# Performance work log

Hardware: AMD Instinct MI355X
Metric: run time of the kernel (lower is better)

The kernel has to match this reference:

```python
import jax, jax.numpy as jnp
import numpy as np
import math

NUM_HEADS = 16
D_MODEL = 1024
B, T = 1, 4096


def setup_inputs() -> dict:
    key = jax.random.key(0)
    kx, kq, kk, kv, ko = jax.random.split(key, 5)
    s = 1.0 / math.sqrt(D_MODEL)
    return {
        "x": jax.random.normal(kx, (B, T, D_MODEL), dtype=jnp.float32),
        "Wq": jax.random.normal(kq, (D_MODEL, D_MODEL), dtype=jnp.float32) * s,
        "Wk": jax.random.normal(kk, (D_MODEL, D_MODEL), dtype=jnp.float32) * s,
        "Wv": jax.random.normal(kv, (D_MODEL, D_MODEL), dtype=jnp.float32) * s,
        "Wo": jax.random.normal(ko, (D_MODEL, D_MODEL), dtype=jnp.float32) * s,
    }


def reference(x, Wq, Wk, Wv, Wo):
    # x: (B, T, D); weights stored torch-Linear style: y = x @ W.T
    Bx, Tx, D = x.shape
    H = NUM_HEADS
    dk = D // H
    q = (x @ Wq.T).reshape(Bx, Tx, H, dk)  # (B,T,H,dk)
    k = (x @ Wk.T).reshape(Bx, Tx, H, dk)
    v = (x @ Wv.T).reshape(Bx, Tx, H, dk)
    # scores: (B,H,T,T), scaled dot-product
    scores = jnp.einsum("bthd,bshd->bhts", q, k) / math.sqrt(dk)
    causal_mask = jnp.triu(jnp.ones((Tx, Tx), dtype=bool), k=1)  # True above diag
    scores = jnp.where(causal_mask, jnp.float32(-jnp.inf), scores).astype(jnp.float32)
    attn = jax.nn.softmax(scores, axis=-1)  # fp32 softmax, as in the torch module
    out = jnp.einsum("bhts,bshd->bthd", attn, v).reshape(Bx, Tx, D)
    return out @ Wo.T
```

## Files before the change

### kernel.cpp

```cpp
#include <hip/hip_runtime.h>
#include <hip/hip_bf16.h>
#include <math.h>

typedef __attribute__((ext_vector_type(8)))  __bf16 bf16x8;
typedef __attribute__((ext_vector_type(4)))  __bf16 bf16x4;
typedef __attribute__((ext_vector_type(4)))  float  f32x4;
typedef __attribute__((ext_vector_type(16))) float  f32x16;

static constexpr int T_SEQ = 4096;
static constexpr int DM    = 1024;
static constexpr int NH    = 16;
static constexpr int C2_QB    = 22;
static constexpr int C3_QB    = 44;
static constexpr int SPL_ROWS = T_SEQ - C2_QB * 64;
static constexpr int C3_ROWS  = T_SEQ - C3_QB * 64;
static constexpr int NY = 126;
static constexpr float QSCALE = 0.125f * 1.44269504088896340736f;
static constexpr float FIXED_M = 10.0f;

__device__ __forceinline__ void gload16(const void* g, void* l) {
    __builtin_amdgcn_global_load_lds(
        (const __attribute__((address_space(1))) unsigned int*)g,
        (__attribute__((address_space(3))) unsigned int*)l,
        16, 0, 0);
}

__device__ __forceinline__ unsigned cvtpk_bf16(float a, float b) {
    unsigned r;
    asm("v_cvt_pk_bf16_f32 %0, %1, %2" : "=v"(r) : "v"(a), "v"(b));
    return r;
}
__device__ __forceinline__ void permswap(unsigned& x, unsigned& y) {
    asm("v_permlane32_swap_b32 %0, %1" : "+v"(x), "+v"(y));
}
__device__ __forceinline__ float xhalf_sum(float v) {
    union { float f; unsigned u; } a, b;
    a.f = v; b.f = v;
    asm volatile("" : "+v"(b.u));
    permswap(a.u, b.u);
    return a.f + b.f;
}

__global__ __launch_bounds__(256)
void cvt_bf16(const float* __restrict__ in, __bf16* __restrict__ out, int n4) {
    int i = blockIdx.x * blockDim.x + threadIdx.x;
    if (i >= n4) return;
    float4 v = ((const float4*)in)[i];
    bf16x4 o;
    o[0] = (__bf16)v.x; o[1] = (__bf16)v.y; o[2] = (__bf16)v.z; o[3] = (__bf16)v.w;
    ((bf16x4*)out)[i] = o;
}

__global__ __launch_bounds__(256)
void cvt4_bf16(const float* __restrict__ a0, const float* __restrict__ a1,
               const float* __restrict__ a2, const float* __restrict__ a3,
               __bf16* __restrict__ o0, __bf16* __restrict__ o1,
               __bf16* __restrict__ o2, __bf16* __restrict__ o3, int n4) {
    int i = blockIdx.x * blockDim.x + threadIdx.x;
    if (i >= n4) return;
    const float* in = blockIdx.y == 0 ? a0 : blockIdx.y == 1 ? a1 : blockIdx.y == 2 ? a2 : a3;
    __bf16* out     = blockIdx.y == 0 ? o0 : blockIdx.y == 1 ? o1 : blockIdx.y == 2 ? o2 : o3;
    float4 v = ((const float4*)in)[i];
    bf16x4 o;
    o[0] = (__bf16)v.x; o[1] = (__bf16)v.y; o[2] = (__bf16)v.z; o[3] = (__bf16)v.w;
    ((bf16x4*)out)[i] = o;
}

template<bool OUT_BF16>
__device__ __forceinline__ void gemm_body(const __bf16* __restrict__ A,
                                          const __bf16* __restrict__ B,
                                          void* __restrict__ Cout,
                                          int N, int K, float scale,
                                          int bx, int by) {
    __shared__ __align__(16) __bf16 Al[128 * 64];
    __shared__ __align__(16) __bf16 Bl[128 * 64];
    const int tid  = threadIdx.x;
    const int lane = tid & 63;
    const int wid  = tid >> 6;
    const int wr   = wid >> 1, wc = wid & 1;
    const int m0   = by * 128, n0 = bx * 128;
    const int r    = lane & 15, g = lane >> 4;

    f32x4 acc[4][4];
    const f32x4 z4 = {0.f, 0.f, 0.f, 0.f};
    #pragma unroll
    for (int i = 0; i < 4; ++i)
        #pragma unroll
        for (int j = 0; j < 4; ++j) acc[i][j] = z4;

    for (int kt = 0; kt < K; kt += 64) {
        __syncthreads();
        #pragma unroll
        for (int p = 0; p < 4; ++p) {
            int u    = p * 256 + tid;
            int row  = u >> 3;
            int col8 = (u & 7) ^ (row & 7);
            gload16(A + (size_t)(m0 + row) * K + kt + col8 * 8,
                    (char*)Al + (p * 256 + wid * 64) * 16);
            gload16(B + (size_t)(n0 + row) * K + kt + col8 * 8,
                    (char*)Bl + (p * 256 + wid * 64) * 16);
        }
        __syncthreads();
        __builtin_amdgcn_s_setprio(1);
        #pragma unroll
        for (int kk = 0; kk < 2; ++kk) {
            bf16x8 af[4], bfr[4];
            #pragma unroll
            for (int mi = 0; mi < 4; ++mi)
                af[mi] = *(const bf16x8*)&Al[(wr * 64 + mi * 16 + r) * 64 + (((kk * 4 + g) ^ (r & 7)) * 8)];
            #pragma unroll
            for (int nj = 0; nj < 4; ++nj)
                bfr[nj] = *(const bf16x8*)&Bl[(wc * 64 + nj * 16 + r) * 64 + (((kk * 4 + g) ^ (r & 7)) * 8)];
            #pragma unroll
            for (int mi = 0; mi < 4; ++mi)
                #pragma unroll
                for (int nj = 0; nj < 4; ++nj)
                    acc[mi][nj] = __builtin_amdgcn_mfma_f32_16x16x32_bf16(af[mi], bfr[nj], acc[mi][nj], 0, 0, 0);
        }
        __builtin_amdgcn_s_setprio(0);
    }
    #pragma unroll
    for (int mi = 0; mi < 4; ++mi)
        #pragma unroll
        for (int nj = 0; nj < 4; ++nj)
            #pragma unroll
            for (int j = 0; j < 4; ++j) {
                int row = m0 + wr * 64 + mi * 16 + g * 4 + j;
                int col = n0 + wc * 64 + nj * 16 + r;
                float v = acc[mi][nj][j] * scale;
                if (OUT_BF16) ((__bf16*)Cout)[(size_t)row * N + col] = (__bf16)v;
                else          ((float*)Cout)[(size_t)row * N + col]  = v;
            }
}

__global__ __launch_bounds__(256)
void gemm_qkv(const __bf16* __restrict__ A,
              const __bf16* __restrict__ W0, const __bf16* __restrict__ W1,
              const __bf16* __restrict__ W2,
              __bf16* __restrict__ O0, __bf16* __restrict__ O1, __bf16* __restrict__ O2) {
    const int z = blockIdx.z;
    const __bf16* B = z == 0 ? W0 : (z == 1 ? W1 : W2);
    __bf16*       C = z == 0 ? O0 : (z == 1 ? O1 : O2);
    float scale = z == 0 ? QSCALE : 1.0f;
    gemm_body<true>(A, B, C, DM, DM, scale, blockIdx.x, blockIdx.y);
}

__global__ __launch_bounds__(256)
void gemm_out(const __bf16* __restrict__ A, const __bf16* __restrict__ B,
              float* __restrict__ C) {
    gemm_body<false>(A, B, C, DM, DM, 1.0f, blockIdx.x, blockIdx.y);
}

__global__ __launch_bounds__(256)
void vtrans(const __bf16* __restrict__ V, __bf16* __restrict__ Vt) {
    __shared__ __bf16 tl[64][72];
    const int tid = threadIdx.x;
    const int t0  = blockIdx.x * 64;
    const int h   = blockIdx.y;
    #pragma unroll
    for (int p = 0; p < 2; ++p) {
        int c = p * 256 + tid, row = c >> 3, col8 = c & 7;
        *(bf16x8*)&tl[row][col8 * 8] =
            *(const bf16x8*)(V + (size_t)(t0 + row) * DM + h * 64 + col8 * 8);
    }
    __syncthreads();
    #pragma unroll
    for (int p = 0; p < 2; ++p) {
        int c = p * 256 + tid, d = c >> 3, tc8 = c & 7;
        bf16x8 o;
        #pragma unroll
        for (int e = 0; e < 8; ++e) o[e] = tl[tc8 * 8 + e][d];
        *(bf16x8*)(Vt + (size_t)(h * 64 + d) * T_SEQ + t0 + tc8 * 8) = o;
    }
}

__global__ __launch_bounds__(128)
void attn_fwd(const __bf16* __restrict__ Q, const __bf16* __restrict__ Kp,
              const __bf16* __restrict__ Vt, __bf16* __restrict__ O,
              __bf16* __restrict__ U0, __bf16* __restrict__ U1,
              __bf16* __restrict__ U2, float* __restrict__ Lb)
{
    __shared__ __align__(16) __bf16 Kl[64 * 64];
    __shared__ __align__(16) __bf16 Vl[64 * 64];
    const int tid  = threadIdx.x;
    const int lane = tid & 63, wid = tid >> 6;
    const int l31  = lane & 31;
    const int hi   = lane >> 5;
    const int h    = blockIdx.x;
    const int y    = blockIdx.y;
    int qb, chunk, nc;
    if (y < 60)       { qb = 63 - y / 3;        chunk = y % 3;        nc = 3; }
    else if (y < 104) { int s = y - 60; qb = 43 - s / 2; chunk = s % 2; nc = 2; }
    else              { qb = 21 - (y - 104);    chunk = 0;            nc = 1; }
    const int n    = qb + 1;
    const int base = n / nc, rem = n % nc;
    const int t0i  = chunk * base + (chunk < rem ? chunk : rem);
    const int t1i  = t0i + base + (chunk < rem ? 1 : 0) - 1;
    const int qw = qb * 64 + wid * 32;
    const int qg = qw + l31;

    bf16x8 qf[4];
    #pragma unroll
    for (int kd0 = 0; kd0 < 4; ++kd0)
        qf[kd0] = *(const bf16x8*)(Q + (size_t)qg * DM + h * 64 + kd0 * 16 + hi * 8);

    float l_i = 0.f;
    f32x16 oacc[2];
    #pragma unroll
    for (int d = 0; d < 2; ++d)
        #pragma unroll
        for (int e = 0; e < 16; ++e) oacc[d][e] = 0.f;

    bf16x8 kreg[4], vreg[4];
    auto stage_lds = [&](int t) {
        #pragma unroll
        for (int p = 0; p < 4; ++p) {
            int u    = p * 128 + tid;
            int row  = u >> 3;
            int col8 = (u & 7) ^ (row & 7);
            gload16(Kp + (size_t)(t * 64 + row) * DM + h * 64 + col8 * 8,
                    (char*)Kl + (p * 128 + wid * 64) * 16);
            gload16(Vt + (size_t)(h * 64 + row) * T_SEQ + t * 64 + col8 * 8,
                    (char*)Vl + (p * 128 + wid * 64) * 16);
        }
    };
    auto ldK = [&](int t) {
        #pragma unroll
        for (int p = 0; p < 4; ++p) {
            int u = p * 128 + tid, row = u >> 3, c = u & 7;
            kreg[p] = *(const bf16x8*)(Kp + (size_t)(t * 64 + row) * DM + h * 64 + c * 8);
        }
    };
    auto ldV = [&](int t) {
        #pragma unroll
        for (int p = 0; p < 4; ++p) {
            int u = p * 128 + tid, row = u >> 3, c = u & 7;
            vreg[p] = *(const bf16x8*)(Vt + (size_t)(h * 64 + row) * T_SEQ + t * 64 + c * 8);
        }
    };
    auto wrK = [&]() {
        #pragma unroll
        for (int p = 0; p < 4; ++p) {
            int u = p * 128 + tid, row = u >> 3, c = u & 7;
            *(bf16x8*)&Kl[(row << 6) + ((c ^ (row & 7)) << 3)] = kreg[p];
        }
    };
    auto wrV = [&]() {
        #pragma unroll
        for (int p = 0; p < 4; ++p) {
            int u = p * 128 + tid, row = u >> 3, c = u & 7;
            *(bf16x8*)&Vl[(row << 6) + ((c ^ (row & 7)) << 3)] = vreg[p];
        }
    };

    auto qk = [&](f32x16* sdst) {
        #pragma unroll
        for (int ksub = 0; ksub < 2; ++ksub) {
            const int row = ksub * 32 + l31;
            f32x16 a;
            #pragma unroll
            for (int e = 0; e < 16; ++e) a[e] = 0.f;
            #pragma unroll
            for (int kd0 = 0; kd0 < 4; ++kd0) {
                bf16x8 kf = *(const bf16x8*)
                    &Kl[(row << 6) + ((((kd0 << 1) + hi) ^ (row & 7)) << 3)];
                a = __builtin_amdgcn_mfma_f32_32x32x16_bf16(kf, qf[kd0], a, 0, 0, 0);
            }
            sdst[ksub] = a;
        }
    };
    auto mask_sf = [&](f32x16* s, int t) {
        const int kb = (t << 6) + 4 * hi;
        #pragma unroll
        for (int ksub = 0; ksub < 2; ++ksub)
            #pragma unroll
            for (int e = 0; e < 16; ++e) {
                int k = kb + ksub * 32 + ((e & 3) + 8 * (e >> 2));
                if (k > qg) s[ksub][e] = -1e30f;
            }
    };

    stage_lds(t0i);
    if (t0i + 1 <= t1i) ldK(t0i + 1);
    __syncthreads();
    f32x16 sf[2], sfn[2];
    qk(sf);
    if (t0i == qb) mask_sf(sf, t0i);
    __syncthreads();
    if (t0i + 1 <= t1i) wrK();
    __syncthreads();

    for (int t = t0i; t <= t1i; ++t) {
        const bool have_next  = (t + 1 <= t1i);
        const bool have_next2 = (t + 2 <= t1i);
        if (have_next2) ldK(t + 2);
        if (have_next)  ldV(t + 1);
        __builtin_amdgcn_s_setprio(1);
        if (have_next) {
            qk(sfn);
            if (t + 1 == qb) mask_sf(sfn, t + 1);
        }
        __builtin_amdgcn_s_setprio(0);
        float p[32];
        #pragma unroll
        for (int i = 0; i < 32; ++i)
            p[i] = exp2f(sf[i >> 4][i & 15] - FIXED_M);
        {
            float s0[8];
            #pragma unroll
            for (int e = 0; e < 8; ++e)
                s0[e] = (p[e] + p[e + 8]) + (p[e + 16] + p[e + 24]);
            #pragma unroll
            for (int s = 4; s > 0; s >>= 1)
                #pragma unroll
                for (int e = 0; e < s; ++e) s0[e] += s0[e + s];
            l_i += xhalf_sum(s0[0]);
        }
        __builtin_amdgcn_s_setprio(1);
        #pragma unroll
        for (int ks = 0; ks < 4; ++ks) {
            unsigned w0 = cvtpk_bf16(p[8 * ks + 0], p[8 * ks + 1]);
            unsigned w1 = cvtpk_bf16(p[8 * ks + 2], p[8 * ks + 3]);
            unsigned w2 = cvtpk_bf16(p[8 * ks + 4], p[8 * ks + 5]);
            unsigned w3 = cvtpk_bf16(p[8 * ks + 6], p[8 * ks + 7]);
            permswap(w0, w2);
            permswap(w1, w3);
            union { unsigned u[4]; bf16x8 v; } pu;
            pu.u[0] = w0; pu.u[1] = w1; pu.u[2] = w2; pu.u[3] = w3;
            #pragma unroll
            for (int dsub = 0; dsub < 2; ++dsub) {
                const int row = dsub * 32 + l31;
                bf16x8 vt = *(const bf16x8*)
                    &Vl[(row << 6) + ((((ks << 1) + hi) ^ (row & 7)) << 3)];
                oacc[dsub] = __builtin_amdgcn_mfma_f32_32x32x16_bf16(vt, pu.v, oacc[dsub], 0, 0, 0);
            }
        }
        __builtin_amdgcn_s_setprio(0);
        if (have_next) {
            __syncthreads();
            if (have_next2) wrK();
            wrV();
            __syncthreads();
        }
        if (have_next) {
            sf[0] = sfn[0];
            sf[1] = sfn[1];
        }
    }
    __syncthreads();
    __bf16* ow = &Kl[0] + wid * 2048;
    const float invl = (nc > 1) ? 1.0f : (1.f / l_i);
    #pragma unroll
    for (int dsub = 0; dsub < 2; ++dsub)
        #pragma unroll
        for (int e = 0; e < 16; ++e) {
            int d = dsub * 32 + ((e & 3) + 8 * (e >> 2)) + 4 * hi;
            float v = oacc[dsub][e] * invl;
            int bo = l31 * 128 + ((2 * d) ^ ((l31 & 7) << 4));
            *(__bf16*)((char*)ow + bo) = (__bf16)v;
        }
    if (nc == 1) {
        #pragma unroll
        for (int i = 0; i < 4; ++i) {
            int u  = hi * 4 + i;
            int bo = l31 * 128 + ((u * 16) ^ ((l31 & 7) << 4));
            bf16x8 v8 = *(const bf16x8*)((char*)ow + bo);
            *(bf16x8*)(O + (size_t)qg * DM + h * 64 + u * 8) = v8;
        }
    } else {
        __bf16* Uc = (chunk == 0) ? U0 : (chunk == 1) ? U1 : U2;
        const int rows  = (chunk == 2) ? C3_ROWS : SPL_ROWS;
        const int ridx  = qg - ((chunk == 2) ? C3_QB * 64 : C2_QB * 64);
        #pragma unroll
        for (int i = 0; i < 4; ++i) {
            int u  = hi * 4 + i;
            int bo = l31 * 128 + ((u * 16) ^ ((l31 & 7) << 4));
            bf16x8 v8 = *(const bf16x8*)((char*)ow + bo);
            *(bf16x8*)(Uc + ((size_t)h * rows + ridx) * 64 + u * 8) = v8;
        }
        if (hi == 0) {
            size_t off = (chunk == 0) ? ((size_t)h * SPL_ROWS + ridx)
                       : (chunk == 1) ? ((size_t)(NH + h) * SPL_ROWS + ridx)
                                      : ((size_t)2 * NH * SPL_ROWS + (size_t)h * C3_ROWS + ridx);
            Lb[off] = l_i;
        }
    }
}

__global__ __launch_bounds__(256)
void attn_combine(const __bf16* __restrict__ U0, const __bf16* __restrict__ U1,
                  const __bf16* __restrict__ U2, const float* __restrict__ Lb,
                  __bf16* __restrict__ O) {
    int gid = blockIdx.x * 256 + threadIdx.x;
    int rh  = gid >> 3;
    int e8  = gid & 7;
    int ridx = rh >> 4, h = rh & 15;
    int qg   = C2_QB * 64 + ridx;
    bool has3 = (qg >= C3_QB * 64);
    float l0 = Lb[(size_t)h * SPL_ROWS + ridx];
    float l1 = Lb[(size_t)(NH + h) * SPL_ROWS + ridx];
    float l2 = has3 ? Lb[(size_t)2 * NH * SPL_ROWS + (size_t)h * C3_ROWS + (qg - C3_QB * 64)] : 0.f;
    float inv = 1.f / (l0 + l1 + l2);
    bf16x8 u0 = *(const bf16x8*)(U0 + ((size_t)h * SPL_ROWS + ridx) * 64 + e8 * 8);
    bf16x8 u1 = *(const bf16x8*)(U1 + ((size_t)h * SPL_ROWS + ridx) * 64 + e8 * 8);
    bf16x8 o;
    if (has3) {
        bf16x8 u2 = *(const bf16x8*)(U2 + ((size_t)h * C3_ROWS + (qg - C3_QB * 64)) * 64 + e8 * 8);
        #pragma unroll
        for (int j = 0; j < 8; ++j)
            o[j] = (__bf16)((((float)u0[j] + (float)u1[j]) + (float)u2[j]) * inv);
    } else {
        #pragma unroll
        for (int j = 0; j < 8; ++j)
            o[j] = (__bf16)(((float)u0[j] + (float)u1[j]) * inv);
    }
    *(bf16x8*)(O + (size_t)qg * DM + h * 64 + e8 * 8) = o;
}

extern "C" void kernel_launch(void* const* d_in, const int* in_sizes, int n_in,
                              void* d_out, int out_size, void* d_ws, size_t ws_size,
                              hipStream_t stream) {
    const float* x  = (const float*)d_in[0];
    const float* Wq = (const float*)d_in[1];
    const float* Wk = (const float*)d_in[2];
    const float* Wv = (const float*)d_in[3];
    const float* Wo = (const float*)d_in[4];
    float* out = (float*)d_out;

    char* ws = (char*)d_ws;
    const size_t MB = (size_t)1 << 20;
    __bf16* xb    = (__bf16*)(ws + 0 * MB);
    __bf16* U0B   = (__bf16*)(ws + 0 * MB);
    __bf16* wqb   = (__bf16*)(ws + 8 * MB);
    float*  LbB   = (float*)(ws + 8 * MB);
    __bf16* wkb   = (__bf16*)(ws + 10 * MB);
    __bf16* U2B   = (__bf16*)(ws + 10 * MB);
    __bf16* wvb   = (__bf16*)(ws + 12 * MB);
    __bf16* wob   = (__bf16*)(ws + 14 * MB);
    __bf16* Qb    = (__bf16*)(ws + 16 * MB);
    __bf16* Kb    = (__bf16*)(ws + 24 * MB);
    __bf16* Vb    = (__bf16*)(ws + 32 * MB);
    __bf16* U1B   = (__bf16*)(ws + 32 * MB);
    __bf16* attnb = (__bf16*)(ws + 40 * MB);
    __bf16* VtR   = (__bf16*)(ws + 48 * MB);

    const int nX = T_SEQ * DM / 4;
    const int nW = DM * DM / 4;
    cvt_bf16<<<(nX + 255) / 256, 256, 0, stream>>>(x, xb, nX);
    cvt4_bf16<<<dim3((nW + 255) / 256, 4), 256, 0, stream>>>(Wq, Wk, Wv, Wo,
                                                             wqb, wkb, wvb, wob, nW);

    gemm_qkv<<<dim3(DM / 128, T_SEQ / 128, 3), 256, 0, stream>>>(xb, wqb, wkb, wvb, Qb, Kb, Vb);

    vtrans<<<dim3(T_SEQ / 64, NH), 256, 0, stream>>>(Vb, VtR);

    attn_fwd<<<dim3(NH, NY), 128, 0, stream>>>(Qb, Kb, VtR, attnb, U0B, U1B, U2B, LbB);

    attn_combine<<<(SPL_ROWS * NH * 8) / 256, 256, 0, stream>>>(U0B, U1B, U2B, LbB, attnb);

    gemm_out<<<dim3(DM / 128, T_SEQ / 128), 256, 0, stream>>>(attnb, wob, out);
}
```

Measured before the change: 186.6 us.

## Double-buffer K and V tiles in LDS for attention pipeline

Replaces the single K/V LDS buffers with two ping-pong buffers and prefetches both K and V two tiles ahead into registers, writing them into the buffer just consumed. V for the next tile is now already resident in LDS when its PV step runs, which removes a staging step from the per-iteration critical path. It also adds a min-blocks hint to launch_bounds. LDS use per block doubles and register pressure rises from holding both K and V prefetches, which can reduce occupancy or force spills.

```diff
diff --git a/kernel.cpp b/kernel.cpp
--- a/kernel.cpp
+++ b/kernel.cpp
@@ -174,14 +174,14 @@
     }
 }
 
-__global__ __launch_bounds__(128)
+__global__ __launch_bounds__(128, 4)
 void attn_fwd(const __bf16* __restrict__ Q, const __bf16* __restrict__ Kp,
               const __bf16* __restrict__ Vt, __bf16* __restrict__ O,
               __bf16* __restrict__ U0, __bf16* __restrict__ U1,
               __bf16* __restrict__ U2, float* __restrict__ Lb)
 {
-    __shared__ __align__(16) __bf16 Kl[64 * 64];
-    __shared__ __align__(16) __bf16 Vl[64 * 64];
+    __shared__ __align__(16) __bf16 Kl[2][64 * 64];
+    __shared__ __align__(16) __bf16 Vl[2][64 * 64];
     const int tid  = threadIdx.x;
     const int lane = tid & 63, wid = tid >> 6;
     const int l31  = lane & 31;
@@ -211,49 +211,23 @@
         #pragma unroll
         for (int e = 0; e < 16; ++e) oacc[d][e] = 0.f;
 
-    bf16x8 kreg[4], vreg[4];
-    auto stage_lds = [&](int t) {
+    auto stage_lds = [&](int t, int buf) {
         #pragma unroll
         for (int p = 0; p < 4; ++p) {
             int u    = p * 128 + tid;
             int row  = u >> 3;
             int col8 = (u & 7) ^ (row & 7);
             gload16(Kp + (size_t)(t * 64 + row) * DM + h * 64 + col8 * 8,
-                    (char*)Kl + (p * 128 + wid * 64) * 16);
+                    (char*)&Kl[buf][0] + (p * 128 + wid * 64) * 16);
             gload16(Vt + (size_t)(h * 64 + row) * T_SEQ + t * 64 + col8 * 8,
-                    (char*)Vl + (p * 128 + wid * 64) * 16);
+                    (char*)&Vl[buf][0] + (p * 128 + wid * 64) * 16);
         }
     };
-    auto ldK = [&](int t) {
-        #pragma unroll
-        for (int p = 0; p < 4; ++p) {
-            int u = p * 128 + tid, row = u >> 3, c = u & 7;
-            kreg[p] = *(const bf16x8*)(Kp + (size_t)(t * 64 + row) * DM + h * 64 + c * 8);
-        }
-    };
-    auto ldV = [&](int t) {
-        #pragma unroll
-        for (int p = 0; p < 4; ++p) {
-            int u = p * 128 + tid, row = u >> 3, c = u & 7;
-            vreg[p] = *(const bf16x8*)(Vt + (size_t)(h * 64 + row) * T_SEQ + t * 64 + c * 8);
-        }
-    };
-    auto wrK = [&]() {
-        #pragma unroll
-        for (int p = 0; p < 4; ++p) {
-            int u = p * 128 + tid, row = u >> 3, c = u & 7;
-            *(bf16x8*)&Kl[(row << 6) + ((c ^ (row & 7)) << 3)] = kreg[p];
-        }
-    };
-    auto wrV = [&]() {
-        #pragma unroll
-        for (int p = 0; p < 4; ++p) {
-            int u = p * 128 + tid, row = u >> 3, c = u & 7;
-            *(bf16x8*)&Vl[(row << 6) + ((c ^ (row & 7)) << 3)] = vreg[p];
-        }
-    };
-
-    auto qk = [&](f32x16* sdst) {
+    stage_lds(t0i, 0);
+    if (t1i > t0i) stage_lds(t0i + 1, 1);
+    __syncthreads();
+
+    auto qk = [&](f32x16* sdst, int buf) {
         #pragma unroll
         for (int ksub = 0; ksub < 2; ++ksub) {
             const int row = ksub * 32 + l31;
@@ -263,7 +237,7 @@
             #pragma unroll
             for (int kd0 = 0; kd0 < 4; ++kd0) {
                 bf16x8 kf = *(const bf16x8*)
-                    &Kl[(row << 6) + ((((kd0 << 1) + hi) ^ (row & 7)) << 3)];
+                    &Kl[buf][(row << 6) + ((((kd0 << 1) + hi) ^ (row & 7)) << 3)];
                 a = __builtin_amdgcn_mfma_f32_32x32x16_bf16(kf, qf[kd0], a, 0, 0, 0);
             }
             sdst[ksub] = a;
@@ -280,24 +254,29 @@
             }
     };
 
-    stage_lds(t0i);
-    if (t0i + 1 <= t1i) ldK(t0i + 1);
-    __syncthreads();
     f32x16 sf[2], sfn[2];
-    qk(sf);
+    qk(sf, 0);
     if (t0i == qb) mask_sf(sf, t0i);
-    __syncthreads();
-    if (t0i + 1 <= t1i) wrK();
-    __syncthreads();
-
+
+    bf16x8 kreg[4], vreg[4];
     for (int t = t0i; t <= t1i; ++t) {
+        const int cur = (t - t0i) & 1;
         const bool have_next  = (t + 1 <= t1i);
         const bool have_next2 = (t + 2 <= t1i);
-        if (have_next2) ldK(t + 2);
-        if (have_next)  ldV(t + 1);
+        if (have_next2) {
+            const int t2 = t + 2;
+            #pragma unroll
+            for (int p = 0; p < 4; ++p) {
+                int u   = p * 128 + tid;
+                int row = u >> 3;
+                int c   = u & 7;
+                kreg[p] = *(const bf16x8*)(Kp + (size_t)(t2 * 64 + row) * DM + h * 64 + c * 8);
+                vreg[p] = *(const bf16x8*)(Vt + (size_t)(h * 64 + row) * T_SEQ + t2 * 64 + c * 8);
+            }
+        }
         __builtin_amdgcn_s_setprio(1);
         if (have_next) {
-            qk(sfn);
+            qk(sfn, cur ^ 1);
             if (t + 1 == qb) mask_sf(sfn, t + 1);
         }
         __builtin_amdgcn_s_setprio(0);
@@ -331,15 +310,21 @@
             for (int dsub = 0; dsub < 2; ++dsub) {
                 const int row = dsub * 32 + l31;
                 bf16x8 vt = *(const bf16x8*)
-                    &Vl[(row << 6) + ((((ks << 1) + hi) ^ (row & 7)) << 3)];
+                    &Vl[cur][(row << 6) + ((((ks << 1) + hi) ^ (row & 7)) << 3)];
                 oacc[dsub] = __builtin_amdgcn_mfma_f32_32x32x16_bf16(vt, pu.v, oacc[dsub], 0, 0, 0);
             }
         }
         __builtin_amdgcn_s_setprio(0);
-        if (have_next) {
+        if (have_next2) {
             __syncthreads();
-            if (have_next2) wrK();
-            wrV();
+            #pragma unroll
+            for (int p = 0; p < 4; ++p) {
+                int u   = p * 128 + tid;
+                int row = u >> 3;
+                int c   = u & 7;
+                *(bf16x8*)&Kl[cur][(row << 6) + ((c ^ (row & 7)) << 3)] = kreg[p];
+                *(bf16x8*)&Vl[cur][(row << 6) + ((c ^ (row & 7)) << 3)] = vreg[p];
+            }
             __syncthreads();
         }
         if (have_next) {
@@ -348,7 +333,7 @@
         }
     }
     __syncthreads();
-    __bf16* ow = &Kl[0] + wid * 2048;
+    __bf16* ow = &Kl[0][0] + wid * 2048;
     const float invl = (nc > 1) ? 1.0f : (1.f / l_i);
     #pragma unroll
     for (int dsub = 0; dsub < 2; ++dsub)
```

After: 196.3 us. 1.05x slower.
